# Kernel tuning notes

Hardware: AMD Instinct MI355X
Metric: run time of the kernel (lower is better)

## Reference

```python
import jax, jax.numpy as jnp
import numpy as np

EPS = 1e-3  # keras BatchNormalization default epsilon
K = 16


def _graph_feature(x, k):
    # x: [B, N, C] -> edge: [B, N, k, 2C]
    sq = jnp.sum(x * x, axis=-1)                       # [B, N]
    # negative squared distance (larger = closer); self is max
    pd = 2.0 * jnp.einsum('bnc,bmc->bnm', x, x) - sq[:, :, None] - sq[:, None, :]
    _, idx = jax.lax.top_k(pd, k)                      # [B, N, k]
    nbr = jax.vmap(lambda xb, ib: xb[ib])(x, idx)      # [B, N, k, C]
    ctr = jnp.broadcast_to(x[:, :, None, :], nbr.shape)
    return jnp.concatenate([ctr, nbr], axis=-1)        # [B, N, k, 2C]


def _bn(y, g, b, m, v):
    return (y - m) * (g * jax.lax.rsqrt(v + EPS)) + b


def _edge_block(x, W, g, b, m, v, k):
    e = _graph_feature(x, k)                           # [B, N, k, 2C]
    h = jnp.einsum('bnkc,cd->bnkd', e, W)              # 1x1 conv, no bias
    h = jax.nn.relu(_bn(h, g, b, m, v))
    return jnp.max(h, axis=2)                          # [B, N, D]


def setup_inputs() -> dict:
    key = jax.random.key(0)
    ks = jax.random.split(key, 32)
    B, N = 8, 2048
    x = jax.random.normal(ks[0], (B, N, 3), dtype=jnp.float32)
    dims = [(6, 64), (128, 64), (128, 128), (256, 256), (512, 512)]
    d = {'x': x}
    for i, (cin, cout) in enumerate(dims):
        j = i + 1
        d[f'W{j}'] = jax.random.normal(ks[1 + i], (cin, cout), dtype=jnp.float32) * (1.0 / np.sqrt(cin))
        d[f'g{j}'] = jax.random.uniform(ks[6 + i], (cout,), dtype=jnp.float32, minval=0.5, maxval=1.5)
        d[f'b{j}'] = jax.random.normal(ks[11 + i], (cout,), dtype=jnp.float32) * 0.1
        d[f'm{j}'] = jax.random.normal(ks[16 + i], (cout,), dtype=jnp.float32) * 0.1
        d[f'v{j}'] = jax.random.uniform(ks[21 + i], (cout,), dtype=jnp.float32, minval=0.5, maxval=1.5)
    return d


def reference(x, W1, g1, b1, m1, v1, W2, g2, b2, m2, v2, W3, g3, b3, m3, v3,
              W4, g4, b4, m4, v4, W5, g5, b5, m5, v5):
    x1 = _edge_block(x,  W1, g1, b1, m1, v1, K)   # [B, N, 64]
    x2 = _edge_block(x1, W2, g2, b2, m2, v2, K)   # [B, N, 64]
    x3 = _edge_block(x2, W3, g3, b3, m3, v3, K)   # [B, N, 128]
    x4 = _edge_block(x3, W4, g4, b4, m4, v4, K)   # [B, N, 256]
    x5 = jnp.concatenate([x1, x2, x3, x4], axis=-1)  # [B, N, 512]
    h5 = jnp.einsum('bnc,cd->bnd', x5, W5)           # 1x1 conv1d, no bias
    return jax.nn.relu(_bn(h5, g5, b5, m5, v5))      # [B, N, 512]
```

## Files before the change

kernel.cpp:

```cpp
#include <hip/hip_runtime.h>

#define NP 2048
#define BTOT 8
#define BN_TOT 16384
#define KC 16
#define NTILE 32
#define NEG_INF (-__builtin_inff())

template <typename JM>
__device__ __forceinline__ void select16(const float (&v)[32], int lane, float* svw,
                                         int* sjw, int* out, int jb, JM jmap) {
  float lmax = v[0];
#pragma unroll
  for (int t = 1; t < 32; ++t) lmax = fmaxf(lmax, v[t]);

  int rank = 0;
  for (int s = 0; s < 64; ++s) {
    float o = __shfl(lmax, s, 64);
    rank += (o > lmax) || (o == lmax && s < lane);
  }
  unsigned long long m15 = __ballot(rank == 15);
  float T0 = __shfl(lmax, (int)__builtin_ctzll(m15), 64);

  unsigned long long lowmask = (1ull << lane) - 1ull;
  unsigned keepmask = 0u;
  int base = 0;
#pragma unroll
  for (int t = 0; t < 32; ++t) {
    bool keep = (v[t] >= T0);
    unsigned long long mk = __ballot(keep);
    if (keep) {
      keepmask |= (1u << t);
      int pos = base + (int)__popcll(mk & lowmask);
      if (pos < 256) { svw[pos] = v[t]; sjw[pos] = jmap(t); }
    }
    base += (int)__popcll(mk);
  }
  int cnt = base;

  if (cnt <= 64) {
    __threadfence_block();
    float mv = NEG_INF;
    int mj = 1 << 30;
    if (lane < cnt) { mv = svw[lane]; mj = sjw[lane]; }
    int rk = 0;
    for (int s = 0; s < 64; ++s) {
      float ov = __shfl(mv, s, 64);
      int oj = __shfl(mj, s, 64);
      rk += (ov > mv) || (ov == mv && oj < mj);
    }
    if (lane < cnt && rk < 16) out[rk] = jb + mj;
    return;
  }

  if (cnt <= 256) {
    __threadfence_block();
    for (int r = 0; r < 16; ++r) {
      float lbv = NEG_INF;
      int lbj = 1 << 30, lbp = -1;
      for (int i = lane; i < cnt; i += 64) {
        float cv = svw[i];
        int cj = sjw[i];
        if (cv > lbv || (cv == lbv && cj < lbj)) { lbv = cv; lbj = cj; lbp = i; }
      }
      float bv = lbv;
      int bj = lbj;
#pragma unroll
      for (int off = 32; off > 0; off >>= 1) {
        float ov = __shfl_xor(bv, off, 64);
        int oj = __shfl_xor(bj, off, 64);
        if (ov > bv || (ov == bv && oj < bj)) { bv = ov; bj = oj; }
      }
      if (lane == 0) out[r] = jb + bj;
      if (lbp >= 0 && lbj == bj) svw[lbp] = NEG_INF;
      __threadfence_block();
    }
    return;
  }

  {
    unsigned avail = keepmask;
    for (int r = 0; r < 16; ++r) {
      float bv = NEG_INF;
      int bj = 1 << 30, bt = -1;
      unsigned am = avail;
      while (am) {
        int t = __builtin_ctz(am);
        am &= am - 1;
        float vv = v[t];
        int jj = jmap(t);
        if (vv > bv || (vv == bv && jj < bj)) { bv = vv; bj = jj; bt = t; }
      }
      float gv = bv;
      int gj = bj;
#pragma unroll
      for (int off = 32; off > 0; off >>= 1) {
        float ov = __shfl_xor(gv, off, 64);
        int oj = __shfl_xor(gj, off, 64);
        if (ov > gv || (ov == gv && oj < gj)) { gv = ov; gj = oj; }
      }
      if (lane == 0) out[r] = jb + gj;
      if (bt >= 0 && bj == gj) avail &= ~(1u << bt);
    }
  }
}

__global__ __launch_bounds__(256) void sqnorm_kernel(const float* __restrict__ X,
                                                     int lda, int C,
                                                     float* __restrict__ sq) {
  int wave = threadIdx.x >> 6, lane = threadIdx.x & 63;
  int row = blockIdx.x * 4 + wave;
  float s = 0.f;
  for (int c = lane; c < C; c += 64) {
    float t = X[(size_t)row * lda + c];
    s += t * t;
  }
#pragma unroll
  for (int off = 32; off > 0; off >>= 1) s += __shfl_xor(s, off, 64);
  if (lane == 0) sq[row] = s;
}

__global__ __launch_bounds__(256) void dist_gemm(const float* __restrict__ X, int lda, int K,
                                                 const float* __restrict__ sq,
                                                 float* __restrict__ pd, int batch0) {
  int bz = blockIdx.z;
  const float* Xb = X + (size_t)(batch0 + bz) * NP * lda;
  const float* sqb = sq + (size_t)(batch0 + bz) * NP;
  float* pdb = pd + (size_t)bz * NP * NP;
  int rem = blockIdx.x, bi = 0;
  while (rem >= NTILE - bi) { rem -= NTILE - bi; ++bi; }
  int bj = bi + rem;
  int i0 = bi * 64, j0 = bj * 64;
  __shared__ float At[KC][68];
  __shared__ float Bt[KC][68];
  int t = threadIdx.x;
  int tx = t & 15, ty = t >> 4;
  int lk = t & 15, lr = t >> 4;
  float acc[4][4] = {};
  for (int k0 = 0; k0 < K; k0 += KC) {
    int kk = k0 + lk;
    bool kv = kk < K;
#pragma unroll
    for (int u = 0; u < 4; ++u) {
      int r = lr + u * 16;
      At[lk][r] = kv ? Xb[(size_t)(i0 + r) * lda + kk] : 0.f;
      Bt[lk][r] = kv ? Xb[(size_t)(j0 + r) * lda + kk] : 0.f;
    }
    __syncthreads();
#pragma unroll
    for (int q = 0; q < KC; ++q) {
      float4 a4 = *(const float4*)&At[q][ty * 4];
      float4 b4 = *(const float4*)&Bt[q][tx * 4];
      float a[4] = {a4.x, a4.y, a4.z, a4.w};
      float bv[4] = {b4.x, b4.y, b4.z, b4.w};
#pragma unroll
      for (int ii = 0; ii < 4; ++ii)
#pragma unroll
        for (int jj = 0; jj < 4; ++jj)
          acc[ii][jj] = fmaf(a[ii], bv[jj], acc[ii][jj]);
    }
    __syncthreads();
  }
  float4 sqj4 = *(const float4*)&sqb[j0 + tx * 4];
#pragma unroll
  for (int ii = 0; ii < 4; ++ii) {
    int i = i0 + ty * 4 + ii;
    float4 o;
    o.x = 2.f * acc[ii][0] - sqj4.x;
    o.y = 2.f * acc[ii][1] - sqj4.y;
    o.z = 2.f * acc[ii][2] - sqj4.z;
    o.w = 2.f * acc[ii][3] - sqj4.w;
    *(float4*)&pdb[(size_t)i * NP + j0 + tx * 4] = o;
  }
  if (bi != bj) {
    float4 sqi4 = *(const float4*)&sqb[i0 + ty * 4];
#pragma unroll
    for (int jj = 0; jj < 4; ++jj) {
      int j = j0 + tx * 4 + jj;
      float4 o;
      o.x = 2.f * acc[0][jj] - sqi4.x;
      o.y = 2.f * acc[1][jj] - sqi4.y;
      o.z = 2.f * acc[2][jj] - sqi4.z;
      o.w = 2.f * acc[3][jj] - sqi4.w;
      *(float4*)&pdb[(size_t)j * NP + i0 + ty * 4] = o;
    }
  }
}

__global__ __launch_bounds__(256) void topk_kernel(const float* __restrict__ pd,
                                                   int* __restrict__ idx_out, int batch0) {
  __shared__ float sv[4][256];
  __shared__ int sj[4][256];
  int wave = threadIdx.x >> 6, lane = threadIdx.x & 63;
  int row = blockIdx.x * 4 + wave;
  const float* prow = pd + (size_t)row * NP;
  int grow = batch0 * NP + row;
  int jb = (grow >> 11) << 11;
  float v[32];
#pragma unroll
  for (int u = 0; u < 8; ++u) {
    float4 q = *(const float4*)&prow[u * 256 + (lane << 2)];
    v[u * 4 + 0] = q.x;
    v[u * 4 + 1] = q.y;
    v[u * 4 + 2] = q.z;
    v[u * 4 + 3] = q.w;
  }
  select16(v, lane, sv[wave], sj[wave], idx_out + (size_t)grow * 16, jb,
           [lane](int t) { return ((t >> 2) << 8) + (lane << 2) + (t & 3); });
}

__global__ __launch_bounds__(256) void dist3_topk(const float* __restrict__ x,
                                                  int* __restrict__ idx_out) {
  __shared__ float4 xs4[NP];
  __shared__ float sv[4][256];
  __shared__ int sj[4][256];
  int wave = threadIdx.x >> 6, lane = threadIdx.x & 63;
  int b = blockIdx.x >> 7;
  int row0 = (blockIdx.x & 127) * 16;
  const float* xb = x + (size_t)b * NP * 3;
  for (int n = threadIdx.x; n < NP; n += 256) {
    float a0 = xb[3 * n], a1 = xb[3 * n + 1], a2 = xb[3 * n + 2];
    xs4[n] = make_float4(a0, a1, a2, a0 * a0 + a1 * a1 + a2 * a2);
  }
  __syncthreads();
  int jb = b << 11;
  for (int rr = 0; rr < 4; ++rr) {
    int row = row0 + wave * 4 + rr;
    float4 c = xs4[row];
    float v[32];
#pragma unroll
    for (int t = 0; t < 32; ++t) {
      int j = lane + t * 64;
      float4 p = xs4[j];
      float dot = c.x * p.x + c.y * p.y + c.z * p.z;
      v[t] = 2.f * dot - p.w;
    }
    select16(v, lane, sv[wave], sj[wave], idx_out + (size_t)(jb + row) * 16, jb,
             [lane](int t) { return lane + t * 64; });
  }
}

__global__ __launch_bounds__(256) void feat_gemm(const float* __restrict__ A, int lda, int K,
                                                 const float* __restrict__ W, int D,
                                                 float* __restrict__ outT,
                                                 float* __restrict__ outB) {
  const float* Wz = W + (size_t)blockIdx.z * K * D;
  float* o = blockIdx.z ? outB : outT;
  int n0 = blockIdx.x * 64, m0 = blockIdx.y * 64;
  __shared__ float At[KC][68];
  __shared__ float Bt[KC][68];
  int t = threadIdx.x;
  int tx = t & 15, ty = t >> 4;
  float acc[4][4] = {};
  for (int k0 = 0; k0 < K; k0 += KC) {
    {
      int lk = t & 15, lr = t >> 4;
      int kk = k0 + lk;
      bool kv = kk < K;
#pragma unroll
      for (int u = 0; u < 4; ++u) {
        int r = lr + u * 16;
        At[lk][r] = kv ? A[(size_t)(m0 + r) * lda + kk] : 0.f;
      }
      int n = t & 63, kq0 = t >> 6;
#pragma unroll
      for (int u = 0; u < 4; ++u) {
        int kq = kq0 + u * 4;
        int kg = k0 + kq;
        Bt[kq][n] = (kg < K) ? Wz[(size_t)kg * D + n0 + n] : 0.f;
      }
    }
    __syncthreads();
#pragma unroll
    for (int q = 0; q < KC; ++q) {
      float4 a4 = *(const float4*)&At[q][ty * 4];
      float4 b4 = *(const float4*)&Bt[q][tx * 4];
      float a[4] = {a4.x, a4.y, a4.z, a4.w};
      float bv[4] = {b4.x, b4.y, b4.z, b4.w};
#pragma unroll
      for (int ii = 0; ii < 4; ++ii)
#pragma unroll
        for (int jj = 0; jj < 4; ++jj)
          acc[ii][jj] = fmaf(a[ii], bv[jj], acc[ii][jj]);
    }
    __syncthreads();
  }
#pragma unroll
  for (int ii = 0; ii < 4; ++ii) {
    float4 o4 = make_float4(acc[ii][0], acc[ii][1], acc[ii][2], acc[ii][3]);
    *(float4*)&o[(size_t)(m0 + ty * 4 + ii) * D + n0 + tx * 4] = o4;
  }
}

__global__ __launch_bounds__(256) void gather_bn_relu(const float* __restrict__ ZT,
                                                      const float* __restrict__ YB,
                                                      const int* __restrict__ idx, int D,
                                                      const float* __restrict__ g,
                                                      const float* __restrict__ bta,
                                                      const float* __restrict__ mu,
                                                      const float* __restrict__ va,
                                                      float* __restrict__ X5, int coff) {
  __shared__ int nb[16];
  int bn = blockIdx.x, d = threadIdx.x;
  if (d < 16) nb[d] = idx[(size_t)bn * 16 + d];
  __syncthreads();
  float mx = NEG_INF;
#pragma unroll
  for (int j = 0; j < 16; ++j) mx = fmaxf(mx, YB[(size_t)nb[j] * D + d]);
  float h = ZT[(size_t)bn * D + d] + mx;
  float s = g[d] / sqrtf(va[d] + 1e-3f);
  float val = (h - mu[d]) * s + bta[d];
  X5[(size_t)bn * 512 + coff + d] = fmaxf(val, 0.f);
}

__global__ __launch_bounds__(256) void final_gemm(const float* __restrict__ A,
                                                  const float* __restrict__ W,
                                                  const float* __restrict__ g,
                                                  const float* __restrict__ bta,
                                                  const float* __restrict__ mu,
                                                  const float* __restrict__ va,
                                                  float* __restrict__ out) {
  const int K = 512, D = 512;
  int n0 = blockIdx.x * 64, m0 = blockIdx.y * 64;
  __shared__ float At[KC][68];
  __shared__ float Bt[KC][68];
  int t = threadIdx.x;
  int tx = t & 15, ty = t >> 4;
  float acc[4][4] = {};
  for (int k0 = 0; k0 < K; k0 += KC) {
    {
      int lk = t & 15, lr = t >> 4;
      int kk = k0 + lk;
#pragma unroll
      for (int u = 0; u < 4; ++u) {
        int r = lr + u * 16;
        At[lk][r] = A[(size_t)(m0 + r) * 512 + kk];
      }
      int n = t & 63, kq0 = t >> 6;
#pragma unroll
      for (int u = 0; u < 4; ++u) {
        int kq = kq0 + u * 4;
        Bt[kq][n] = W[(size_t)(k0 + kq) * D + n0 + n];
      }
    }
    __syncthreads();
#pragma unroll
    for (int q = 0; q < KC; ++q) {
      float4 a4 = *(const float4*)&At[q][ty * 4];
      float4 b4 = *(const float4*)&Bt[q][tx * 4];
      float a[4] = {a4.x, a4.y, a4.z, a4.w};
      float bv[4] = {b4.x, b4.y, b4.z, b4.w};
#pragma unroll
      for (int ii = 0; ii < 4; ++ii)
#pragma unroll
        for (int jj = 0; jj < 4; ++jj)
          acc[ii][jj] = fmaf(a[ii], bv[jj], acc[ii][jj]);
    }
    __syncthreads();
  }
  float sc[4], tc[4];
#pragma unroll
  for (int jj = 0; jj < 4; ++jj) {
    int col = n0 + tx * 4 + jj;
    float s = g[col] / sqrtf(va[col] + 1e-3f);
    sc[jj] = s;
    tc[jj] = bta[col] - mu[col] * s;
  }
#pragma unroll
  for (int ii = 0; ii < 4; ++ii) {
    float4 o4;
    o4.x = fmaxf(acc[ii][0] * sc[0] + tc[0], 0.f);
    o4.y = fmaxf(acc[ii][1] * sc[1] + tc[1], 0.f);
    o4.z = fmaxf(acc[ii][2] * sc[2] + tc[2], 0.f);
    o4.w = fmaxf(acc[ii][3] * sc[3] + tc[3], 0.f);
    *(float4*)&out[(size_t)(m0 + ty * 4 + ii) * 512 + n0 + tx * 4] = o4;
  }
}

extern "C" void kernel_launch(void* const* d_in, const int* in_sizes, int n_in,
                              void* d_out, int out_size, void* d_ws, size_t ws_size,
                              hipStream_t stream) {
  const float* x = (const float*)d_in[0];
  const float *W[5], *g[5], *bt[5], *mu[5], *va[5];
  for (int j = 0; j < 5; ++j) {
    W[j] = (const float*)d_in[1 + j * 5 + 0];
    g[j] = (const float*)d_in[1 + j * 5 + 1];
    bt[j] = (const float*)d_in[1 + j * 5 + 2];
    mu[j] = (const float*)d_in[1 + j * 5 + 3];
    va[j] = (const float*)d_in[1 + j * 5 + 4];
  }
  char* p = (char*)d_ws;
  float* X5 = (float*)p; p += (size_t)BN_TOT * 512 * 4;
  float* ZT = (float*)p; p += (size_t)BN_TOT * 256 * 4;
  float* YB = (float*)p; p += (size_t)BN_TOT * 256 * 4;
  int* idx = (int*)p;    p += (size_t)BN_TOT * 16 * 4;
  float* sq = (float*)p; p += (size_t)BN_TOT * 4;
  float* pd = (float*)p;
  size_t used = (size_t)(p - (char*)d_ws);
  size_t pdcap = (ws_size > used) ? (ws_size - used) / ((size_t)NP * NP * 4) : 0;
  int nb = (int)(pdcap < 1 ? 1 : (pdcap > (size_t)BTOT ? (size_t)BTOT : pdcap));

  struct Blk { const float* A; int lda, C, D, coff, w; };
  Blk blks[4] = {
      {x, 3, 3, 64, 0, 0},
      {X5 + 0, 512, 64, 64, 64, 1},
      {X5 + 64, 512, 64, 128, 128, 2},
      {X5 + 128, 512, 128, 256, 256, 3},
  };
  for (int q = 0; q < 4; ++q) {
    Blk& B = blks[q];
    if (q == 0) {
      dist3_topk<<<1024, 256, 0, stream>>>(x, idx);
    } else {
      sqnorm_kernel<<<BN_TOT / 4, 256, 0, stream>>>(B.A, B.lda, B.C, sq);
      for (int b0 = 0; b0 < BTOT; b0 += nb) {
        int cnt = (BTOT - b0 < nb) ? (BTOT - b0) : nb;
        dist_gemm<<<dim3(NTILE * (NTILE + 1) / 2, 1, cnt), 256, 0, stream>>>(
            B.A, B.lda, B.C, sq, pd, b0);
        topk_kernel<<<cnt * NP / 4, 256, 0, stream>>>(pd, idx, b0);
      }
    }
    feat_gemm<<<dim3(B.D / 64, BN_TOT / 64, 2), 256, 0, stream>>>(
        B.A, B.lda, B.C, W[B.w], B.D, ZT, YB);
    gather_bn_relu<<<BN_TOT, B.D, 0, stream>>>(ZT, YB, idx, B.D, g[B.w], bt[B.w], mu[B.w],
                                               va[B.w], X5, B.coff);
  }
  final_gemm<<<dim3(512 / 64, BN_TOT / 64), 256, 0, stream>>>(X5, W[4], g[4], bt[4], mu[4],
                                                              va[4], (float*)d_out);
}
```

Before: 684.7 us.

## Run final 512x512 GEMM on bf16 MFMA with split-bf16 three-term emulation

After: 634.3 us. 7.4% less time.

```diff
diff --git a/kernel.cpp b/kernel.cpp
--- a/kernel.cpp
+++ b/kernel.cpp
@@ -7,13 +7,26 @@
 #define NTILE 32
 #define NEG_INF (-__builtin_inff())
 
+typedef __attribute__((ext_vector_type(8))) short short8;
+typedef __attribute__((ext_vector_type(4))) float f32x4;
+
+__device__ __forceinline__ unsigned short bf16_rne(float x) {
+  unsigned u = __float_as_uint(x);
+  u += 0x7FFFu + ((u >> 16) & 1u);
+  return (unsigned short)(u >> 16);
+}
+__device__ __forceinline__ void split2(float x, unsigned short& h, unsigned short& l) {
+  h = bf16_rne(x);
+  float hf = __uint_as_float((unsigned)h << 16);
+  l = bf16_rne(x - hf);
+}
+
 template <typename JM>
 __device__ __forceinline__ void select16(const float (&v)[32], int lane, float* svw,
                                          int* sjw, int* out, int jb, JM jmap) {
   float lmax = v[0];
 #pragma unroll
   for (int t = 1; t < 32; ++t) lmax = fmaxf(lmax, v[t]);
-
   int rank = 0;
   for (int s = 0; s < 64; ++s) {
     float o = __shfl(lmax, s, 64);
@@ -313,67 +326,120 @@
   X5[(size_t)bn * 512 + coff + d] = fmaxf(val, 0.f);
 }
 
-__global__ __launch_bounds__(256) void final_gemm(const float* __restrict__ A,
-                                                  const float* __restrict__ W,
+__global__ __launch_bounds__(256) void split_x5(const float* __restrict__ X5,
+                                                unsigned short* __restrict__ Xh,
+                                                unsigned short* __restrict__ Xl) {
+  const int total4 = BN_TOT * 512 / 4;
+  for (int i = blockIdx.x * 256 + threadIdx.x; i < total4; i += gridDim.x * 256) {
+    float4 v = *(const float4*)&X5[i * 4];
+    ushort4 h, l;
+    split2(v.x, h.x, l.x);
+    split2(v.y, h.y, l.y);
+    split2(v.z, h.z, l.z);
+    split2(v.w, h.w, l.w);
+    *(ushort4*)&Xh[i * 4] = h;
+    *(ushort4*)&Xl[i * 4] = l;
+  }
+}
+
+__global__ __launch_bounds__(256) void w5t_split(const float* __restrict__ W5,
+                                                 unsigned short* __restrict__ Wh,
+                                                 unsigned short* __restrict__ Wl) {
+  int n = blockIdx.x;
+  for (int k = threadIdx.x; k < 512; k += 256) {
+    unsigned short h, l;
+    split2(W5[(size_t)k * 512 + n], h, l);
+    Wh[(size_t)n * 512 + k] = h;
+    Wl[(size_t)n * 512 + k] = l;
+  }
+}
+
+__global__ __launch_bounds__(256) void final_mfma(const unsigned short* __restrict__ Ah,
+                                                  const unsigned short* __restrict__ Al,
+                                                  const unsigned short* __restrict__ Bh,
+                                                  const unsigned short* __restrict__ Bl,
                                                   const float* __restrict__ g,
                                                   const float* __restrict__ bta,
                                                   const float* __restrict__ mu,
                                                   const float* __restrict__ va,
                                                   float* __restrict__ out) {
-  const int K = 512, D = 512;
-  int n0 = blockIdx.x * 64, m0 = blockIdx.y * 64;
-  __shared__ float At[KC][68];
-  __shared__ float Bt[KC][68];
-  int t = threadIdx.x;
-  int tx = t & 15, ty = t >> 4;
-  float acc[4][4] = {};
-  for (int k0 = 0; k0 < K; k0 += KC) {
-    {
-      int lk = t & 15, lr = t >> 4;
-      int kk = k0 + lk;
-#pragma unroll
-      for (int u = 0; u < 4; ++u) {
-        int r = lr + u * 16;
-        At[lk][r] = A[(size_t)(m0 + r) * 512 + kk];
-      }
-      int n = t & 63, kq0 = t >> 6;
-#pragma unroll
-      for (int u = 0; u < 4; ++u) {
-        int kq = kq0 + u * 4;
-        Bt[kq][n] = W[(size_t)(k0 + kq) * D + n0 + n];
-      }
-    }
-    __syncthreads();
-#pragma unroll
-    for (int q = 0; q < KC; ++q) {
-      float4 a4 = *(const float4*)&At[q][ty * 4];
-      float4 b4 = *(const float4*)&Bt[q][tx * 4];
-      float a[4] = {a4.x, a4.y, a4.z, a4.w};
-      float bv[4] = {b4.x, b4.y, b4.z, b4.w};
-#pragma unroll
-      for (int ii = 0; ii < 4; ++ii)
-#pragma unroll
-        for (int jj = 0; jj < 4; ++jj)
-          acc[ii][jj] = fmaf(a[ii], bv[jj], acc[ii][jj]);
-    }
-    __syncthreads();
-  }
-  float sc[4], tc[4];
-#pragma unroll
-  for (int jj = 0; jj < 4; ++jj) {
-    int col = n0 + tx * 4 + jj;
+  int tid = threadIdx.x;
+  int wave = tid >> 6, lane = tid & 63;
+  int wm = wave >> 1, wn = wave & 1;
+  int ln = lane & 15, quad = lane >> 4;
+  int m_base = blockIdx.y * 128 + wm * 64;
+  int n_base = blockIdx.x * 128 + wn * 64;
+
+  f32x4 acc[4][4];
+#pragma unroll
+  for (int i = 0; i < 4; ++i)
+#pragma unroll
+    for (int j = 0; j < 4; ++j) acc[i][j] = (f32x4){0.f, 0.f, 0.f, 0.f};
+
+  size_t aoff[4], boff[4];
+#pragma unroll
+  for (int t = 0; t < 4; ++t) {
+    aoff[t] = (size_t)(m_base + t * 16 + ln) * 512 + quad * 8;
+    boff[t] = (size_t)(n_base + t * 16 + ln) * 512 + quad * 8;
+  }
+
+  short8 cAh[4], cAl[4], cBh[4], cBl[4];
+#pragma unroll
+  for (int t = 0; t < 4; ++t) {
+    cAh[t] = *(const short8*)(Ah + aoff[t]);
+    cAl[t] = *(const short8*)(Al + aoff[t]);
+    cBh[t] = *(const short8*)(Bh + boff[t]);
+    cBl[t] = *(const short8*)(Bl + boff[t]);
+  }
+
+  for (int kk = 0; kk < 16; ++kk) {
+    short8 nAh[4], nAl[4], nBh[4], nBl[4];
+    if (kk < 15) {
+      int ko = (kk + 1) * 32;
+#pragma unroll
+      for (int t = 0; t < 4; ++t) {
+        nAh[t] = *(const short8*)(Ah + aoff[t] + ko);
+        nAl[t] = *(const short8*)(Al + aoff[t] + ko);
+        nBh[t] = *(const short8*)(Bh + boff[t] + ko);
+        nBl[t] = *(const short8*)(Bl + boff[t] + ko);
+      }
+    }
+#pragma unroll
+    for (int tm = 0; tm < 4; ++tm)
+#pragma unroll
+      for (int tn = 0; tn < 4; ++tn) {
+        acc[tm][tn] = __builtin_amdgcn_mfma_f32_16x16x32_bf16(cAh[tm], cBh[tn],
+                                                              acc[tm][tn], 0, 0, 0);
+        acc[tm][tn] = __builtin_amdgcn_mfma_f32_16x16x32_bf16(cAh[tm], cBl[tn],
+                                                              acc[tm][tn], 0, 0, 0);
+        acc[tm][tn] = __builtin_amdgcn_mfma_f32_16x16x32_bf16(cAl[tm], cBh[tn],
+                                                              acc[tm][tn], 0, 0, 0);
+      }
+    if (kk < 15) {
+#pragma unroll
+      for (int t = 0; t < 4; ++t) {
+        cAh[t] = nAh[t];
+        cAl[t] = nAl[t];
+        cBh[t] = nBh[t];
+        cBl[t] = nBl[t];
+      }
+    }
+  }
+
+#pragma unroll
+  for (int tn = 0; tn < 4; ++tn) {
+    int col = n_base + tn * 16 + ln;
     float s = g[col] / sqrtf(va[col] + 1e-3f);
-    sc[jj] = s;
-    tc[jj] = bta[col] - mu[col] * s;
-  }
-#pragma unroll
-  for (int ii = 0; ii < 4; ++ii) {
-    float4 o4;
-    o4.x = fmaxf(acc[ii][0] * sc[0] + tc[0], 0.f);
-    o4.y = fmaxf(acc[ii][1] * sc[1] + tc[1], 0.f);
-    o4.z = fmaxf(acc[ii][2] * sc[2] + tc[2], 0.f);
-    o4.w = fmaxf(acc[ii][3] * sc[3] + tc[3], 0.f);
-    *(float4*)&out[(size_t)(m0 + ty * 4 + ii) * 512 + n0 + tx * 4] = o4;
+    float tc = bta[col] - mu[col] * s;
+#pragma unroll
+    for (int tm = 0; tm < 4; ++tm) {
+      int mrow = m_base + tm * 16 + quad * 4;
+#pragma unroll
+      for (int r = 0; r < 4; ++r) {
+        float val = acc[tm][tn][r] * s + tc;
+        out[(size_t)(mrow + r) * 512 + col] = fmaxf(val, 0.f);
+      }
+    }
   }
 }
 
@@ -395,10 +461,16 @@
   float* YB = (float*)p; p += (size_t)BN_TOT * 256 * 4;
   int* idx = (int*)p;    p += (size_t)BN_TOT * 16 * 4;
   float* sq = (float*)p; p += (size_t)BN_TOT * 4;
+  unsigned short* X5h = (unsigned short*)p; p += (size_t)BN_TOT * 512 * 2;
+  unsigned short* X5l = (unsigned short*)p; p += (size_t)BN_TOT * 512 * 2;
+  unsigned short* W5h = (unsigned short*)p; p += (size_t)512 * 512 * 2;
+  unsigned short* W5l = (unsigned short*)p; p += (size_t)512 * 512 * 2;
   float* pd = (float*)p;
   size_t used = (size_t)(p - (char*)d_ws);
   size_t pdcap = (ws_size > used) ? (ws_size - used) / ((size_t)NP * NP * 4) : 0;
   int nb = (int)(pdcap < 1 ? 1 : (pdcap > (size_t)BTOT ? (size_t)BTOT : pdcap));
+
+  w5t_split<<<512, 256, 0, stream>>>(W[4], W5h, W5l);
 
   struct Blk { const float* A; int lda, C, D, coff, w; };
   Blk blks[4] = {
@@ -425,6 +497,7 @@
     gather_bn_relu<<<BN_TOT, B.D, 0, stream>>>(ZT, YB, idx, B.D, g[B.w], bt[B.w], mu[B.w],
                                                va[B.w], X5, B.coff);
   }
-  final_gemm<<<dim3(512 / 64, BN_TOT / 64), 256, 0, stream>>>(X5, W[4], g[4], bt[4], mu[4],
-                                                              va[4], (float*)d_out);
-}
+  split_x5<<<1024, 256, 0, stream>>>(X5, X5h, X5l);
+  final_mfma<<<dim3(4, 128), 256, 0, stream>>>(X5h, X5l, W5h, W5l, g[4], bt[4], mu[4],
+                                               va[4], (float*)d_out);
+}
```
